# Kernel tuning notes

Measured on AMD Instinct MI355X. Metric: run time of the kernel, lower is better.

## Reference

```python
import jax, jax.numpy as jnp
import numpy as np

N, E, D, L = 50000, 250000, 300, 5
ATOM_V, BOND_V = 128, 16
BN_EPS = 1e-5


def setup_inputs() -> dict:
    key = jax.random.key(0)
    ks = jax.random.split(key, 16)
    inp = {
        'x': jax.random.randint(ks[0], (N, 9), 0, ATOM_V),
        'edge_index': jax.random.randint(ks[1], (2, E), 0, N),
        'edge_attr': jax.random.randint(ks[2], (E, 3), 0, BOND_V),
        # learned parameters
        'atom_emb': jax.random.normal(ks[3], (9, ATOM_V, D), jnp.float32) * 0.02,
        'bond_emb': jax.random.normal(ks[4], (L, 3, BOND_V, D), jnp.float32) * 0.02,
        'eps': jnp.zeros((L,), jnp.float32),
        'W1': jax.random.normal(ks[5], (L, D, 2 * D), jnp.float32) / np.sqrt(D),
        'b1': jnp.zeros((L, 2 * D), jnp.float32),
        'g1': jnp.ones((L, 2 * D), jnp.float32),
        'be1': jnp.zeros((L, 2 * D), jnp.float32),
        'W2': jax.random.normal(ks[6], (L, 2 * D, D), jnp.float32) / np.sqrt(2 * D),
        'b2': jnp.zeros((L, D), jnp.float32),
        'gamma': jnp.ones((L, D), jnp.float32),
        'beta': jnp.zeros((L, D), jnp.float32),
    }
    return inp


def _bn(h, g, b):
    m = h.mean(0)
    v = h.var(0)
    return (h - m) * jax.lax.rsqrt(v + BN_EPS) * g + b


def reference(x, edge_index, edge_attr, atom_emb, bond_emb, eps, W1, b1, g1, be1, W2, b2, gamma, beta):
    src, dst = edge_index[0], edge_index[1]
    # AtomEncoder: sum of per-column embeddings -> [N, D]
    h = atom_emb[jnp.arange(9)[:, None], x.T].sum(0)
    for l in range(L):
        # BondEncoder for this layer -> [E, D]
        e = bond_emb[l][jnp.arange(3)[:, None], edge_attr.T].sum(0)
        # GIN: gather -> relu message -> scatter-add
        msg = jax.nn.relu(h[src] + e)
        agg = jax.ops.segment_sum(msg, dst, num_segments=N)
        z = (1.0 + eps[l]) * h + agg
        # MLP: Linear -> BN -> ReLU -> Linear
        z = jax.nn.relu(_bn(z @ W1[l] + b1[l], g1[l], be1[l])) @ W2[l] + b2[l]
        # outer BatchNorm
        h = _bn(z, gamma[l], beta[l])
        if l < L - 1:
            h = jax.nn.relu(h)
    return h  # JK='last'
```

## Files before the change

kernel.cpp:

```cpp
#include <hip/hip_runtime.h>

#define N_NODES 50000
#define N_EDGES 250000
#define DIM 300
#define DIM2 600
#define NL 5
#define MPAD 50048
#define KP1 320
#define KP2 608
#define NP1 640
#define NP2 384
#define SCAN_BLOCKS 196
#define CT_STRIDE 136

typedef __attribute__((ext_vector_type(8))) _Float16 half8;
typedef __attribute__((ext_vector_type(2))) _Float16 half2v;
typedef __attribute__((ext_vector_type(8))) short short8;
typedef __attribute__((ext_vector_type(4))) float f32x4;
typedef unsigned short ushort;
typedef unsigned int uint;

#define AS1 __attribute__((address_space(1)))
#define AS3 __attribute__((address_space(3)))

static __device__ __forceinline__ ushort f2h(float f) {
    _Float16 h = (_Float16)f;
    return __builtin_bit_cast(ushort, h);
}
static __device__ __forceinline__ float h2f(ushort s) {
    return (float)__builtin_bit_cast(_Float16, s);
}
static __device__ __forceinline__ uint pk2(float a, float b) {
    return (uint)f2h(a) | ((uint)f2h(b) << 16);
}
static __device__ __forceinline__ half2v u2h2(uint u) {
    return __builtin_bit_cast(half2v, u);
}

static __device__ __forceinline__ int xcd_swizzle(int o, int nwg) {
    int q = nwg >> 3, r = nwg & 7;
    int xcd = o & 7, idx = o >> 3;
    return (xcd < r ? xcd * (q + 1) : r * (q + 1) + (xcd - r) * q) + idx;
}

__global__ void atom_enc(const int* __restrict__ x, const float* __restrict__ emb,
                         ushort* __restrict__ h) {
    int idx = blockIdx.x * blockDim.x + threadIdx.x;
    const int PAIRS = DIM / 2;
    if (idx >= N_NODES * PAIRS) return;
    int n = idx / PAIRS, p = idx - n * PAIRS;
    const int* xr = x + n * 9;
    float s0 = 0.f, s1 = 0.f;
#pragma unroll
    for (int i = 0; i < 9; i++) {
        const float2 v = *(const float2*)(emb + (size_t)(i * 128 + xr[i]) * DIM + 2 * p);
        s0 += v.x; s1 += v.y;
    }
    ((uint*)h)[idx] = pk2(s0, s1);
}

__global__ void deg_count(const int* __restrict__ ei, int* __restrict__ deg) {
    int e = blockIdx.x * blockDim.x + threadIdx.x;
    if (e < N_EDGES) atomicAdd(&deg[ei[N_EDGES + e]], 1);
}

__global__ void block_sums(const int* __restrict__ deg, int* __restrict__ bsum) {
    __shared__ int red[256];
    int tid = threadIdx.x;
    int node = blockIdx.x * 256 + tid;
    red[tid] = (node < N_NODES) ? deg[node] : 0;
    __syncthreads();
    for (int off = 128; off > 0; off >>= 1) {
        if (tid < off) red[tid] += red[tid + off];
        __syncthreads();
    }
    if (tid == 0) bsum[blockIdx.x] = red[0];
}

__global__ void scan_bsums(int* __restrict__ bsum) {
    __shared__ int s[256];
    int tid = threadIdx.x;
    int orig = (tid < SCAN_BLOCKS) ? bsum[tid] : 0;
    s[tid] = orig;
    __syncthreads();
    for (int off = 1; off < 256; off <<= 1) {
        int v = (tid >= off) ? s[tid - off] : 0;
        __syncthreads();
        s[tid] += v;
        __syncthreads();
    }
    if (tid < SCAN_BLOCKS) bsum[tid] = s[tid] - orig;
}

__global__ void write_rowstart(const int* __restrict__ deg, const int* __restrict__ bsum,
                               int* __restrict__ rowstart, int* __restrict__ cursor) {
    __shared__ int s[256];
    int tid = threadIdx.x;
    int node = blockIdx.x * 256 + tid;
    int d = (node < N_NODES) ? deg[node] : 0;
    s[tid] = d;
    __syncthreads();
    for (int off = 1; off < 256; off <<= 1) {
        int v = (tid >= off) ? s[tid - off] : 0;
        __syncthreads();
        s[tid] += v;
        __syncthreads();
    }
    int excl = s[tid] - d + bsum[blockIdx.x];
    if (node < N_NODES) {
        rowstart[node] = excl;
        cursor[node] = excl;
    }
    if (blockIdx.x == 0 && tid == 0) rowstart[N_NODES] = N_EDGES;
}

__global__ void csr_fill(const int* __restrict__ ei, const int* __restrict__ ea,
                         int* __restrict__ cursor, int2* __restrict__ epack) {
    int e = blockIdx.x * blockDim.x + threadIdx.x;
    if (e < N_EDGES) {
        int d = ei[N_EDGES + e];
        int slot = atomicAdd(&cursor[d], 1);
        int attr = ea[3 * e] | (ea[3 * e + 1] << 8) | (ea[3 * e + 2] << 16);
        epack[slot] = make_int2(ei[e], attr);
    }
}

__global__ void bond_conv(const float* __restrict__ bond, ushort* __restrict__ bondh) {
    int idx = blockIdx.x * blockDim.x + threadIdx.x;
    if (idx >= 48 * (DIM / 2)) return;
    float2 v = *(const float2*)(bond + 2 * idx);
    ((uint*)bondh)[idx] = pk2(v.x, v.y);
}

__global__ void init_bn(float* __restrict__ scale, float* __restrict__ shift) {
    int i = blockIdx.x * blockDim.x + threadIdx.x;
    if (i < DIM) { scale[i] = 1.f; shift[i] = 0.f; }
}

__launch_bounds__(256)
__global__ void agg_combine(const int* __restrict__ rowstart, const int2* __restrict__ epack,
                            const ushort* __restrict__ bondh, const ushort* __restrict__ h,
                            const float* __restrict__ scale, const float* __restrict__ shift,
                            int relu, const float* __restrict__ epsp, int layer,
                            ushort* __restrict__ A1) {
    int node = blockIdx.x * 4 + (threadIdx.x >> 6);
    int lane = threadIdx.x & 63;
    if (node >= MPAD) return;
    uint* row32 = (uint*)(A1 + (size_t)node * KP1);
    if (node >= N_NODES) {
        for (int i = lane; i < KP1 / 2; i += 64) row32[i] = 0;
        return;
    }
    const int PAIRS = DIM / 2;
    float2 scf[3], shf[3];
    half2v sch[3], shh[3];
#pragma unroll
    for (int i = 0; i < 3; i++) {
        int p = lane + 64 * i;
        scf[i] = make_float2(0.f, 0.f);
        shf[i] = make_float2(0.f, 0.f);
        if (p < PAIRS) {
            scf[i] = *(const float2*)(scale + 2 * p);
            shf[i] = *(const float2*)(shift + 2 * p);
        }
        sch[i] = half2v{(_Float16)scf[i].x, (_Float16)scf[i].y};
        shh[i] = half2v{(_Float16)shf[i].x, (_Float16)shf[i].y};
    }
    float epsv = 1.0f + epsp[layer];
    const uint* hd = (const uint*)(h + (size_t)node * DIM);
    float ax[3], ay[3];
#pragma unroll
    for (int i = 0; i < 3; i++) {
        int p = lane + 64 * i;
        ax[i] = 0.f; ay[i] = 0.f;
        if (p < PAIRS) {
            uint u = hd[p];
            float vx = h2f((ushort)(u & 0xffffu)) * scf[i].x + shf[i].x;
            float vy = h2f((ushort)(u >> 16)) * scf[i].y + shf[i].y;
            if (relu) { vx = fmaxf(vx, 0.f); vy = fmaxf(vy, 0.f); }
            ax[i] = epsv * vx; ay[i] = epsv * vy;
        }
    }

    auto edge_contrib = [&](int2 pk) {
        const uint* hs = (const uint*)(h + (size_t)pk.x * DIM);
        int a0 = pk.y & 0xff, a1v = (pk.y >> 8) & 0xff, a2 = (pk.y >> 16) & 0xff;
        const uint* t0 = (const uint*)(bondh + a0 * DIM);
        const uint* t1 = (const uint*)(bondh + (16 + a1v) * DIM);
        const uint* t2 = (const uint*)(bondh + (32 + a2) * DIM);
        const half2v z = {};
#pragma unroll
        for (int i = 0; i < 3; i++) {
            int p = lane + 64 * i;
            if (p < PAIRS) {
                half2v hv = u2h2(hs[p]) * sch[i] + shh[i];
                if (relu) hv = __builtin_elementwise_max(hv, z);
                half2v m = hv + u2h2(t0[p]) + u2h2(t1[p]) + u2h2(t2[p]);
                m = __builtin_elementwise_max(m, z);
                ax[i] += (float)m.x;
                ay[i] += (float)m.y;
            }
        }
    };

    int e0 = rowstart[node], e1 = rowstart[node + 1];
    int t = e0;
    for (; t + 1 < e1; t += 2) {
        int2 p0 = epack[t];
        int2 p1 = epack[t + 1];
        edge_contrib(p0);
        edge_contrib(p1);
    }
    if (t < e1) edge_contrib(epack[t]);

#pragma unroll
    for (int i = 0; i < 3; i++) {
        int p = lane + 64 * i;
        if (p < KP1 / 2) row32[p] = (p < PAIRS) ? pk2(ax[i], ay[i]) : 0u;
    }
}

__global__ void wt_conv(const float* __restrict__ W, ushort* __restrict__ Wt,
                        int K, int Nc, int KP, int NP) {
    int idx = blockIdx.x * blockDim.x + threadIdx.x;
    if (idx >= KP * NP) return;
    int k = idx / NP, n = idx - k * NP;
    ushort v = 0;
    if (k < K && n < Nc) v = f2h(W[(size_t)k * Nc + n]);
    Wt[(size_t)n * KP + k] = v;
}

__global__ void wt_conv2(const float* __restrict__ W, const float* __restrict__ scale,
                         ushort* __restrict__ Wt) {
    int idx = blockIdx.x * blockDim.x + threadIdx.x;
    if (idx >= KP2 * NP2) return;
    int k = idx / NP2, n = idx - k * NP2;
    ushort v = 0;
    if (k < DIM2 && n < DIM) v = f2h(scale[k] * W[(size_t)k * DIM + n]);
    Wt[(size_t)n * KP2 + k] = v;
}

__launch_bounds__(256)
__global__ void gemm_mfma(const ushort* __restrict__ A, const ushort* __restrict__ Wt,
                          const float* __restrict__ bias, ushort* __restrict__ Cout,
                          int M, int KP, int Nc, int strideC, int ntiles,
                          float* __restrict__ csum, float* __restrict__ csq) {
    __shared__ ushort smem[64 * CT_STRIDE];
    __shared__ float s_sum[128], s_sq[128];
    ushort* As = smem;
    ushort* Bs = smem + 4096;

    int tid = threadIdx.x;
    int w = tid >> 6, lane = tid & 63;
    int quad = lane >> 4, lr = lane & 15;
    int wm = w >> 1, wn = w & 1;
    int wg = xcd_swizzle(blockIdx.x, gridDim.x);
    int m0 = (wg / ntiles) * 128;
    int n0 = (wg % ntiles) * 128;

    if (tid < 128) { s_sum[tid] = 0.f; s_sq[tid] = 0.f; }

    const int kchunk = ((lane & 3) ^ ((lane >> 3) & 3)) * 8;
    const int grow = lane >> 2;
    const ushort* Abase = A + (size_t)m0 * KP + kchunk;
    const ushort* Bbase = Wt + (size_t)n0 * KP + kchunk;
    const int xq = (quad ^ ((lr >> 1) & 3)) * 8;

    f32x4 acc[4][4] = {};

    for (int k0 = 0; k0 < KP; k0 += 32) {
#pragma unroll
        for (int c = w; c < 8; c += 4)
            __builtin_amdgcn_global_load_lds((const AS1 void*)(Abase + (size_t)(16 * c + grow) * KP + k0),
                                             (AS3 void*)(As + c * 512), 16, 0, 0);
#pragma unroll
        for (int c = w; c < 8; c += 4)
            __builtin_amdgcn_global_load_lds((const AS1 void*)(Bbase + (size_t)(16 * c + grow) * KP + k0),
                                             (AS3 void*)(Bs + c * 512), 16, 0, 0);
        __syncthreads();

        half8 a[4], b[4];
#pragma unroll
        for (int mf = 0; mf < 4; mf++)
            a[mf] = __builtin_bit_cast(half8, *(const short8*)(As + (64 * wm + 16 * mf + lr) * 32 + xq));
#pragma unroll
        for (int nf = 0; nf < 4; nf++)
            b[nf] = __builtin_bit_cast(half8, *(const short8*)(Bs + (64 * wn + 16 * nf + lr) * 32 + xq));
        __builtin_amdgcn_s_setprio(1);
#pragma unroll
        for (int mf = 0; mf < 4; mf++)
#pragma unroll
            for (int nf = 0; nf < 4; nf++)
                acc[mf][nf] = __builtin_amdgcn_mfma_f32_16x16x32_f16(a[mf], b[nf], acc[mf][nf], 0, 0, 0);
        __builtin_amdgcn_s_setprio(0);
        __syncthreads();
    }

#pragma unroll
    for (int half = 0; half < 2; half++) {
        if (wm == half) {
#pragma unroll
            for (int nf = 0; nf < 4; nf++) {
                int lcol = 64 * wn + 16 * nf + lr;
                int gn = n0 + lcol;
                float bv = (gn < Nc) ? bias[gn] : 0.f;
                float ps = 0.f, pq = 0.f;
#pragma unroll
                for (int mf = 0; mf < 4; mf++) {
#pragma unroll
                    for (int r = 0; r < 4; r++) {
                        int lrow = 16 * mf + quad * 4 + r;
                        float v = acc[mf][nf][r] + bv;
                        smem[lrow * CT_STRIDE + lcol] = f2h(v);
                        if (m0 + 64 * half + lrow < M && gn < Nc) { ps += v; pq += v * v; }
                    }
                }
                if (gn < Nc) {
                    atomicAdd(&s_sum[lcol], ps);
                    atomicAdd(&s_sq[lcol], pq);
                }
            }
        }
        __syncthreads();
#pragma unroll
        for (int it = 0; it < 4; it++) {
            int idx = tid + it * 256;
            int row = idx >> 4, ch = idx & 15;
            int gcol = n0 + ch * 8;
            if (gcol < Nc) {
                *(short8*)(Cout + (size_t)(m0 + 64 * half + row) * strideC + gcol) =
                    *(const short8*)(smem + row * CT_STRIDE + ch * 8);
            }
        }
        __syncthreads();
    }

    if (tid < 128) {
        int gn = n0 + tid;
        if (gn < Nc) {
            atomicAdd(&csum[gn], s_sum[tid]);
            atomicAdd(&csq[gn], s_sq[tid]);
        }
    }
}

__launch_bounds__(256)
__global__ void gemm2_fused(const ushort* __restrict__ yh, const ushort* __restrict__ Wt,
                            const ushort* __restrict__ t1h, const float* __restrict__ bias,
                            ushort* __restrict__ hout,
                            float* __restrict__ csum, float* __restrict__ csq) {
    __shared__ ushort smem[64 * CT_STRIDE];
    __shared__ ushort s_t[KP2];
    __shared__ float s_sum[128], s_sq[128];
    ushort* As = smem;
    ushort* Bs = smem + 4096;

    int tid = threadIdx.x;
    int w = tid >> 6, lane = tid & 63;
    int quad = lane >> 4, lr = lane & 15;
    int wm = w >> 1, wn = w & 1;
    int wg = xcd_swizzle(blockIdx.x, gridDim.x);
    int m0 = (wg / 3) * 128;
    int n0 = (wg % 3) * 128;

    int r0 = tid >> 2;
    int q = tid & 3;
    int cc = q * 8;
    const int aslot = (q ^ ((r0 >> 1) & 3)) * 8;

    const int kchunk = ((lane & 3) ^ ((lane >> 3) & 3)) * 8;
    const int grow = lane >> 2;
    const ushort* Bbase = Wt + (size_t)n0 * KP2 + kchunk;
    const int xq = (quad ^ ((lr >> 1) & 3)) * 8;

    const ushort* yrow0 = yh + (size_t)(m0 + r0) * DIM2 + cc;
    const ushort* yrow1 = yh + (size_t)(m0 + r0 + 64) * DIM2 + cc;

    if (tid < 128) { s_sum[tid] = 0.f; s_sq[tid] = 0.f; }
    for (int i = tid; i < KP2 / 2; i += 256) ((uint*)s_t)[i] = ((const uint*)t1h)[i];
    __syncthreads();

    f32x4 acc[4][4] = {};
    const int nk = KP2 >> 5;

    for (int t = 0; t < nk; ++t) {
        int k0 = t << 5;
#pragma unroll
        for (int c = w; c < 8; c += 4)
            __builtin_amdgcn_global_load_lds((const AS1 void*)(Bbase + (size_t)(16 * c + grow) * KP2 + k0),
                                             (AS3 void*)(Bs + c * 512), 16, 0, 0);
        int col = k0 + cc;
        half8 a0 = {}, a1 = {};
        if (col < DIM2) {
            half8 tt = *(const half8*)(s_t + col);
            half8 y0 = *(const half8*)(yrow0 + k0);
            half8 y1 = *(const half8*)(yrow1 + k0);
            half8 z = {};
            a0 = __builtin_elementwise_max(y0 + tt, z);
            a1 = __builtin_elementwise_max(y1 + tt, z);
        }
        *(short8*)(As + r0 * 32 + aslot) = __builtin_bit_cast(short8, a0);
        *(short8*)(As + (r0 + 64) * 32 + aslot) = __builtin_bit_cast(short8, a1);
        __syncthreads();

        half8 a[4], b[4];
#pragma unroll
        for (int mf = 0; mf < 4; mf++)
            a[mf] = __builtin_bit_cast(half8, *(const short8*)(As + (64 * wm + 16 * mf + lr) * 32 + xq));
#pragma unroll
        for (int nf = 0; nf < 4; nf++)
            b[nf] = __builtin_bit_cast(half8, *(const short8*)(Bs + (64 * wn + 16 * nf + lr) * 32 + xq));
        __builtin_amdgcn_s_setprio(1);
#pragma unroll
        for (int mf = 0; mf < 4; mf++)
#pragma unroll
            for (int nf = 0; nf < 4; nf++)
                acc[mf][nf] = __builtin_amdgcn_mfma_f32_16x16x32_f16(a[mf], b[nf], acc[mf][nf], 0, 0, 0);
        __builtin_amdgcn_s_setprio(0);
        __syncthreads();
    }

#pragma unroll
    for (int half = 0; half < 2; half++) {
        if (wm == half) {
#pragma unroll
            for (int nf = 0; nf < 4; nf++) {
                int lcol = 64 * wn + 16 * nf + lr;
                int gn = n0 + lcol;
                float bv = (gn < DIM) ? bias[gn] : 0.f;
                float ps = 0.f, pq = 0.f;
#pragma unroll
                for (int mf = 0; mf < 4; mf++) {
#pragma unroll
                    for (int r = 0; r < 4; r++) {
                        int lrow = 16 * mf + quad * 4 + r;
                        float v = acc[mf][nf][r] + bv;
                        smem[lrow * CT_STRIDE + lcol] = f2h(v);
                        if (m0 + 64 * half + lrow < N_NODES && gn < DIM) { ps += v; pq += v * v; }
                    }
                }
                if (gn < DIM) {
                    atomicAdd(&s_sum[lcol], ps);
                    atomicAdd(&s_sq[lcol], pq);
                }
            }
        }
        __syncthreads();
#pragma unroll
        for (int it = 0; it < 8; it++) {
            int idx = tid + it * 256;
            int row = idx >> 5, ch = idx & 31;
            int gm = m0 + 64 * half + row, gcol = n0 + ch * 4;
            if (gm < N_NODES && gcol < DIM) {
                *(uint2*)(hout + (size_t)gm * DIM + gcol) =
                    *(const uint2*)(smem + row * CT_STRIDE + ch * 4);
            }
        }
        __syncthreads();
    }

    if (tid < 128) {
        int gn = n0 + tid;
        if (gn < DIM) {
            atomicAdd(&csum[gn], s_sum[tid]);
            atomicAdd(&csq[gn], s_sq[tid]);
        }
    }
}

__global__ void bn_finalize(const float* __restrict__ sum, const float* __restrict__ sq,
                            const float* __restrict__ g, const float* __restrict__ b,
                            float* __restrict__ scale, float* __restrict__ shift,
                            ushort* __restrict__ th, int n, int npad) {
    int i = blockIdx.x * blockDim.x + threadIdx.x;
    if (i >= n) {
        if (th && i < npad) th[i] = 0;
        return;
    }
    const float invN = 1.0f / (float)N_NODES;
    float m = sum[i] * invN;
    float v = sq[i] * invN - m * m;
    float inv = rsqrtf(v + 1e-5f);
    float sc = g[i] * inv;
    scale[i] = sc;
    shift[i] = b[i] - m * sc;
    if (th) th[i] = f2h((b[i] - m * sc) / sc);
}

__global__ void bn_apply_out(const ushort* __restrict__ h, const float* __restrict__ scale,
                             const float* __restrict__ shift, float* __restrict__ out) {
    int idx = blockIdx.x * blockDim.x + threadIdx.x;
    const int PAIRS = DIM / 2;
    if (idx >= N_NODES * PAIRS) return;
    int p = idx % PAIRS;
    uint u = ((const uint*)h)[idx];
    float2 sc = *(const float2*)(scale + 2 * p);
    float2 sh = *(const float2*)(shift + 2 * p);
    float2 o;
    o.x = h2f((ushort)(u & 0xffffu)) * sc.x + sh.x;
    o.y = h2f((ushort)(u >> 16)) * sc.y + sh.y;
    *(float2*)(out + 2 * idx) = o;
}

extern "C" void kernel_launch(void* const* d_in, const int* in_sizes, int n_in,
                              void* d_out, int out_size, void* d_ws, size_t ws_size,
                              hipStream_t stream) {
    const int* x = (const int*)d_in[0];
    const int* ei = (const int*)d_in[1];
    const int* ea = (const int*)d_in[2];
    const float* atom_emb = (const float*)d_in[3];
    const float* bond_emb = (const float*)d_in[4];
    const float* eps = (const float*)d_in[5];
    const float* W1 = (const float*)d_in[6];
    const float* b1 = (const float*)d_in[7];
    const float* g1 = (const float*)d_in[8];
    const float* be1 = (const float*)d_in[9];
    const float* W2 = (const float*)d_in[10];
    const float* b2 = (const float*)d_in[11];
    const float* gamma = (const float*)d_in[12];
    const float* beta = (const float*)d_in[13];
    float* out = (float*)d_out;

    float* ws = (float*)d_ws;
    ushort* h    = (ushort*)ws;
    ushort* A1h  = (ushort*)(ws + 7500000);
    ushort* yh   = (ushort*)(ws + 15507680);
    ushort* Wt1  = (ushort*)(ws + 30522080);
    ushort* Wt2  = (ushort*)(ws + 30624480);
    ushort* bondh = (ushort*)(ws + 30741216);
    float* stats = ws + 30748416;
    ushort* t1h  = (ushort*)(ws + 30752016);
    int* rowstart = (int*)(ws + 30752320);
    int* deg      = rowstart + 50001;
    int* cursor   = deg + 50000;
    int2* epack   = (int2*)(cursor + 50000 + 1);
    int* bsum     = (int*)(epack + 250000);

    float* sum1 = stats;
    float* sq1  = stats + 600;
    float* sum2 = stats + 1200;
    float* sq2  = stats + 1500;
    float* scale1 = stats + 1800;
    float* shift1 = stats + 2400;
    float* scale2 = stats + 3000;
    float* shift2 = stats + 3300;

    const int PAIRS_N = N_NODES * (DIM / 2);

    hipMemsetAsync(deg, 0, 50000 * sizeof(int), stream);
    deg_count<<<(N_EDGES + 255) / 256, 256, 0, stream>>>(ei, deg);
    block_sums<<<SCAN_BLOCKS, 256, 0, stream>>>(deg, bsum);
    scan_bsums<<<1, 256, 0, stream>>>(bsum);
    write_rowstart<<<SCAN_BLOCKS, 256, 0, stream>>>(deg, bsum, rowstart, cursor);
    csr_fill<<<(N_EDGES + 255) / 256, 256, 0, stream>>>(ei, ea, cursor, epack);

    atom_enc<<<(PAIRS_N + 255) / 256, 256, 0, stream>>>(x, atom_emb, h);
    init_bn<<<(DIM + 255) / 256, 256, 0, stream>>>(scale2, shift2);

    for (int l = 0; l < NL; ++l) {
        hipMemsetAsync(stats, 0, 1800 * sizeof(float), stream);

        bond_conv<<<(48 * (DIM / 2) + 255) / 256, 256, 0, stream>>>(
            bond_emb + (size_t)l * 3 * 16 * DIM, bondh);

        agg_combine<<<(MPAD + 3) / 4, 256, 0, stream>>>(rowstart, epack, bondh,
                                                        h, scale2, shift2, (l > 0) ? 1 : 0,
                                                        eps, l, A1h);

        wt_conv<<<(KP1 * NP1 + 255) / 256, 256, 0, stream>>>(W1 + (size_t)l * DIM * DIM2, Wt1,
                                                             DIM, DIM2, KP1, NP1);

        gemm_mfma<<<(MPAD / 128) * (NP1 / 128), 256, 0, stream>>>(
            A1h, Wt1, b1 + l * DIM2, yh, N_NODES, KP1, DIM2, DIM2, NP1 / 128, sum1, sq1);

        bn_finalize<<<(KP2 + 255) / 256, 256, 0, stream>>>(sum1, sq1, g1 + l * DIM2,
                                                           be1 + l * DIM2, scale1, shift1,
                                                           t1h, DIM2, KP2);

        wt_conv2<<<(KP2 * NP2 + 255) / 256, 256, 0, stream>>>(W2 + (size_t)l * DIM2 * DIM,
                                                              scale1, Wt2);

        gemm2_fused<<<(MPAD / 128) * (NP2 / 128), 256, 0, stream>>>(
            yh, Wt2, t1h, b2 + l * DIM, h, sum2, sq2);

        bn_finalize<<<(DIM + 255) / 256, 256, 0, stream>>>(sum2, sq2, gamma + l * DIM,
                                                           beta + l * DIM, scale2, shift2,
                                                           nullptr, DIM, DIM);
    }

    bn_apply_out<<<(PAIRS_N + 255) / 256, 256, 0, stream>>>(h, scale2, shift2, out);
}
```

Before: 1.160 ms.

## Double-buffer LDS tiles in both GEMM kernels with prefetch two k-steps ahead

Both MFMA GEMM kernels now use two LDS buffers, issuing global-to-LDS loads for k-tile t+2 while computing tile t. Manual s_waitcnt and raw barriers replace __syncthreads. In the fused second GEMM, the y-row loads and bias+ReLU A-tile preparation for the next step also overlap the current MFMAs. Launch bounds now request 4 blocks per CU. The goal is to hide global load latency behind MFMA work, at the cost of double the LDS footprint and fragile hand-written wait counts.

```diff
diff --git a/kernel.cpp b/kernel.cpp
--- a/kernel.cpp
+++ b/kernel.cpp
@@ -22,6 +22,12 @@
 
 #define AS1 __attribute__((address_space(1)))
 #define AS3 __attribute__((address_space(3)))
+
+#define BARRIER() do { \
+    asm volatile("" ::: "memory"); \
+    __builtin_amdgcn_s_barrier(); \
+    asm volatile("" ::: "memory"); \
+} while (0)
 
 static __device__ __forceinline__ ushort f2h(float f) {
     _Float16 h = (_Float16)f;
@@ -240,15 +246,13 @@
     Wt[(size_t)n * KP2 + k] = v;
 }
 
-__launch_bounds__(256)
+__launch_bounds__(256, 4)
 __global__ void gemm_mfma(const ushort* __restrict__ A, const ushort* __restrict__ Wt,
                           const float* __restrict__ bias, ushort* __restrict__ Cout,
                           int M, int KP, int Nc, int strideC, int ntiles,
                           float* __restrict__ csum, float* __restrict__ csq) {
-    __shared__ ushort smem[64 * CT_STRIDE];
+    __shared__ ushort smem[16384];
     __shared__ float s_sum[128], s_sq[128];
-    ushort* As = smem;
-    ushort* Bs = smem + 4096;
 
     int tid = threadIdx.x;
     int w = tid >> 6, lane = tid & 63;
@@ -266,19 +270,29 @@
     const ushort* Bbase = Wt + (size_t)n0 * KP + kchunk;
     const int xq = (quad ^ ((lr >> 1) & 3)) * 8;
 
-    f32x4 acc[4][4] = {};
-
-    for (int k0 = 0; k0 < KP; k0 += 32) {
+    auto stage = [&](int k0, int buf) {
+        ushort* dA = smem + buf * 8192;
 #pragma unroll
         for (int c = w; c < 8; c += 4)
             __builtin_amdgcn_global_load_lds((const AS1 void*)(Abase + (size_t)(16 * c + grow) * KP + k0),
-                                             (AS3 void*)(As + c * 512), 16, 0, 0);
+                                             (AS3 void*)(dA + c * 512), 16, 0, 0);
 #pragma unroll
         for (int c = w; c < 8; c += 4)
             __builtin_amdgcn_global_load_lds((const AS1 void*)(Bbase + (size_t)(16 * c + grow) * KP + k0),
-                                             (AS3 void*)(Bs + c * 512), 16, 0, 0);
-        __syncthreads();
-
+                                             (AS3 void*)(dA + 4096 + c * 512), 16, 0, 0);
+    };
+
+    f32x4 acc[4][4] = {};
+    const int nk = KP >> 5;
+
+    stage(0, 0);
+    stage(32, 1);
+    asm volatile("s_waitcnt vmcnt(4)" ::: "memory");
+    BARRIER();
+
+    for (int t = 0; t < nk; ++t) {
+        const ushort* As = smem + (t & 1) * 8192;
+        const ushort* Bs = As + 4096;
         half8 a[4], b[4];
 #pragma unroll
         for (int mf = 0; mf < 4; mf++)
@@ -286,6 +300,11 @@
 #pragma unroll
         for (int nf = 0; nf < 4; nf++)
             b[nf] = __builtin_bit_cast(half8, *(const short8*)(Bs + (64 * wn + 16 * nf + lr) * 32 + xq));
+        asm volatile("s_waitcnt lgkmcnt(0)" ::: "memory");
+        BARRIER();
+
+        if (t + 2 < nk) stage((t + 2) << 5, t & 1);
+
         __builtin_amdgcn_s_setprio(1);
 #pragma unroll
         for (int mf = 0; mf < 4; mf++)
@@ -293,7 +312,10 @@
             for (int nf = 0; nf < 4; nf++)
                 acc[mf][nf] = __builtin_amdgcn_mfma_f32_16x16x32_f16(a[mf], b[nf], acc[mf][nf], 0, 0, 0);
         __builtin_amdgcn_s_setprio(0);
-        __syncthreads();
+
+        if (t + 2 < nk)       { asm volatile("s_waitcnt vmcnt(4)" ::: "memory"); }
+        else if (t + 1 < nk)  { asm volatile("s_waitcnt vmcnt(0)" ::: "memory"); }
+        BARRIER();
     }
 
 #pragma unroll
@@ -344,16 +366,14 @@
     }
 }
 
-__launch_bounds__(256)
+__launch_bounds__(256, 4)
 __global__ void gemm2_fused(const ushort* __restrict__ yh, const ushort* __restrict__ Wt,
                             const ushort* __restrict__ t1h, const float* __restrict__ bias,
                             ushort* __restrict__ hout,
                             float* __restrict__ csum, float* __restrict__ csq) {
-    __shared__ ushort smem[64 * CT_STRIDE];
+    __shared__ ushort smem[16384];
     __shared__ ushort s_t[KP2];
     __shared__ float s_sum[128], s_sq[128];
-    ushort* As = smem;
-    ushort* Bs = smem + 4096;
 
     int tid = threadIdx.x;
     int w = tid >> 6, lane = tid & 63;
@@ -376,33 +396,49 @@
     const ushort* yrow0 = yh + (size_t)(m0 + r0) * DIM2 + cc;
     const ushort* yrow1 = yh + (size_t)(m0 + r0 + 64) * DIM2 + cc;
 
+    auto stageB = [&](int k0, int buf) {
+        ushort* dB = smem + buf * 8192 + 4096;
+#pragma unroll
+        for (int c = w; c < 8; c += 4)
+            __builtin_amdgcn_global_load_lds((const AS1 void*)(Bbase + (size_t)(16 * c + grow) * KP2 + k0),
+                                             (AS3 void*)(dB + c * 512), 16, 0, 0);
+    };
+
     if (tid < 128) { s_sum[tid] = 0.f; s_sq[tid] = 0.f; }
+
     for (int i = tid; i < KP2 / 2; i += 256) ((uint*)s_t)[i] = ((const uint*)t1h)[i];
-    __syncthreads();
+    half8 y0 = *(const half8*)(yrow0);
+    half8 y1 = *(const half8*)(yrow1);
+    stageB(0, 0);
+    stageB(32, 1);
+    asm volatile("s_waitcnt lgkmcnt(0)" ::: "memory");
+    BARRIER();
+    {
+        half8 z = {};
+        half8 tt = *(const half8*)(s_t + cc);
+        half8 a0 = __builtin_elementwise_max(y0 + tt, z);
+        half8 a1 = __builtin_elementwise_max(y1 + tt, z);
+        *(short8*)(smem + r0 * 32 + aslot) = __builtin_bit_cast(short8, a0);
+        *(short8*)(smem + (r0 + 64) * 32 + aslot) = __builtin_bit_cast(short8, a1);
+    }
+    asm volatile("s_waitcnt vmcnt(2) lgkmcnt(0)" ::: "memory");
+    BARRIER();
 
     f32x4 acc[4][4] = {};
     const int nk = KP2 >> 5;
 
     for (int t = 0; t < nk; ++t) {
-        int k0 = t << 5;
-#pragma unroll
-        for (int c = w; c < 8; c += 4)
-            __builtin_amdgcn_global_load_lds((const AS1 void*)(Bbase + (size_t)(16 * c + grow) * KP2 + k0),
-                                             (AS3 void*)(Bs + c * 512), 16, 0, 0);
-        int col = k0 + cc;
-        half8 a0 = {}, a1 = {};
-        if (col < DIM2) {
-            half8 tt = *(const half8*)(s_t + col);
-            half8 y0 = *(const half8*)(yrow0 + k0);
-            half8 y1 = *(const half8*)(yrow1 + k0);
-            half8 z = {};
-            a0 = __builtin_elementwise_max(y0 + tt, z);
-            a1 = __builtin_elementwise_max(y1 + tt, z);
-        }
-        *(short8*)(As + r0 * 32 + aslot) = __builtin_bit_cast(short8, a0);
-        *(short8*)(As + (r0 + 64) * 32 + aslot) = __builtin_bit_cast(short8, a1);
-        __syncthreads();
-
+        half8 yn0 = {}, yn1 = {};
+        if (t + 1 < nk) {
+            int coln = ((t + 1) << 5) + cc;
+            if (coln < DIM2) {
+                yn0 = *(const half8*)(yrow0 + ((t + 1) << 5));
+                yn1 = *(const half8*)(yrow1 + ((t + 1) << 5));
+            }
+        }
+
+        const ushort* As = smem + (t & 1) * 8192;
+        const ushort* Bs = As + 4096;
         half8 a[4], b[4];
 #pragma unroll
         for (int mf = 0; mf < 4; mf++)
@@ -410,6 +446,11 @@
 #pragma unroll
         for (int nf = 0; nf < 4; nf++)
             b[nf] = __builtin_bit_cast(half8, *(const short8*)(Bs + (64 * wn + 16 * nf + lr) * 32 + xq));
+        asm volatile("s_waitcnt lgkmcnt(0)" ::: "memory");
+        BARRIER();
+
+        if (t + 2 < nk) stageB((t + 2) << 5, t & 1);
+
         __builtin_amdgcn_s_setprio(1);
 #pragma unroll
         for (int mf = 0; mf < 4; mf++)
@@ -417,7 +458,18 @@
             for (int nf = 0; nf < 4; nf++)
                 acc[mf][nf] = __builtin_amdgcn_mfma_f32_16x16x32_f16(a[mf], b[nf], acc[mf][nf], 0, 0, 0);
         __builtin_amdgcn_s_setprio(0);
-        __syncthreads();
+
+        if (t + 1 < nk) {
+            half8 z = {};
+            half8 tt = *(const half8*)(s_t + ((t + 1) << 5) + cc);
+            half8 a0 = __builtin_elementwise_max(yn0 + tt, z);
+            half8 a1 = __builtin_elementwise_max(yn1 + tt, z);
+            ushort* Anx = smem + ((t + 1) & 1) * 8192;
+            *(short8*)(Anx + r0 * 32 + aslot) = __builtin_bit_cast(short8, a0);
+            *(short8*)(Anx + (r0 + 64) * 32 + aslot) = __builtin_bit_cast(short8, a1);
+        }
+        asm volatile("s_waitcnt lgkmcnt(0)" ::: "memory");
+        BARRIER();
     }
 
 #pragma unroll
```

Result: faster. 1.098 ms (-5.3%).
